# Kernel tuning notes

Hardware: AMD Instinct MI355X
Metric: run time of the kernel (lower is better)

## Reference

```python
import jax, jax.numpy as jnp
import numpy as np

B, S = 512, 256          # batch, seq_len
C, H = 8, 16             # num_cells, expert hidden size
M = 20                   # memory_size (hard-coded in module)
NT = C * H               # num_trajectories = 128
ENC_IN = M * (NT + 1)    # 20*129 = 2580, memory_encode input dim
A_H = 16                 # agent LSTM hidden


def setup_inputs() -> dict:
    key = jax.random.key(0)
    ks = jax.random.split(key, 20)
    r = lambda i, shape: 0.1 * jax.random.normal(ks[i], shape, dtype=jnp.float32)
    return {
        "x": jax.random.normal(ks[0], (B, S, 1), dtype=jnp.float32),
        "pred0": jax.random.uniform(ks[1], (B, 1), dtype=jnp.float32),
        "gate0": jax.nn.softmax(jax.random.uniform(ks[2], (B, C), dtype=jnp.float32), axis=1),
        # experts: C parallel LSTM cells (input 1, hidden H) + per-cell scalar head
        "W_ih": r(3, (C, 4 * H, 1)), "W_hh": r(4, (C, 4 * H, H)),
        "b_ih": r(5, (C, 4 * H)), "b_hh": r(6, (C, 4 * H)),
        "W_o": r(7, (C, H)), "b_o": r(8, (C,)),
        # memory_encode: Linear(2580,64) ReLU Linear(64,16) ReLU
        "W1": r(9, (64, ENC_IN)), "b1": r(10, (64,)),
        "W2": r(11, (16, 64)), "b2": r(12, (16,)),
        # gate_linear: Linear(16, C) + softmax
        "Wg": r(13, (C, 16)), "bg": r(14, (C,)),
        # agent: 2 stacked LSTM cells (16 -> 16)
        "Wa_ih": r(15, (2, 4 * A_H, A_H)), "Wa_hh": r(16, (2, 4 * A_H, A_H)),
        "ba_ih": r(17, (2, 4 * A_H)), "ba_hh": r(18, (2, 4 * A_H)),
    }


def _cell(z, c):
    # PyTorch LSTMCell gate order: i, f, g, o
    i, f, g, o = jnp.split(z, 4, axis=-1)
    c2 = jax.nn.sigmoid(f) * c + jax.nn.sigmoid(i) * jnp.tanh(g)
    return jax.nn.sigmoid(o) * jnp.tanh(c2), c2


def reference(x, pred0, gate0, W_ih, W_hh, b_ih, b_hh, W_o, b_o,
              W1, b1, W2, b2, Wg, bg, Wa_ih, Wa_hh, ba_ih, ba_hh):
    mem0 = jnp.zeros((B, M, NT + 1), jnp.float32).at[:, :, -1].set(0.5)
    eh0 = jnp.zeros((B, H), jnp.float32)   # combined expert h (shared across cells)
    a0 = jnp.zeros((2, B, A_H), jnp.float32)

    def step(carry, x_t):
        mem, eh, ec, pred, gate_state, ah, ac = carry
        error = x_t - pred                                        # [B,1]
        # experts: C LSTM cells, all reading the shared combined state
        z = (jnp.einsum('bf,cgf->bcg', x_t, W_ih)
             + jnp.einsum('bh,cgh->bcg', eh, W_hh)
             + b_ih + b_hh)                                       # [B,C,4H]
        nh, nc = _cell(z, ec[:, None, :])                          # [B,C,H]
        o = jnp.einsum('bch,ch->bc', nh, W_o) + b_o               # [B,C]
        # memory_step: matmul(mstep, mem) shifts rows down by 1, row 0 <- w
        w = jnp.concatenate([nh.reshape(B, -1), error], axis=1)   # [B,NT+1]
        mem = jnp.concatenate([w[:, None, :], mem[:, :-1, :]], axis=1)
        # memory_encode MLP
        e1 = jax.nn.relu(mem.reshape(B, -1) @ W1.T + b1)
        ai = jax.nn.relu(e1 @ W2.T + b2)                           # [B,16]
        # agent: 2 stacked LSTM cells
        ah_l, ac_l, inp_l = [], [], ai
        for l in range(2):
            zl = inp_l @ Wa_ih[l].T + ba_ih[l] + ah[l] @ Wa_hh[l].T + ba_hh[l]
            hl, cl = _cell(zl, ac[l])
            ah_l.append(hl); ac_l.append(cl)
            inp_l = hl
        ah2, ac2 = jnp.stack(ah_l), jnp.stack(ac_l)
        gate = jax.nn.softmax(inp_l @ Wg.T + bg, axis=1)           # [B,C]
        # theta = clip(2.5 * mean|mem[:, :10, -1]|, 0, 1)  (relu(t)-relu(t-1))
        theta = jnp.clip(jnp.mean(jnp.abs(mem[:, :10, -1]), axis=1) * 2.5, 0.0, 1.0)[:, None]
        gate = gate * theta + gate_state * (1.0 - theta)
        eh2 = jnp.einsum('bc,bch->bh', gate, nh)                   # bmm(gate, h)
        ec2 = jnp.einsum('bc,bch->bh', gate, nc)
        pred2 = jnp.einsum('bc,bc->b', gate, o)[:, None]           # [B,1]
        return (mem, eh2, ec2, pred2, gate, ah2, ac2), pred2

    xs = jnp.swapaxes(x, 0, 1)  # [S,B,1]
    _, preds = jax.lax.scan(step, (mem0, eh0, eh0, pred0, gate0, a0, a0), xs)
    return jnp.swapaxes(preds, 0, 1)  # [B,S,1]
```

## Files before the change

kernel.cpp:

```cpp
#include <hip/hip_runtime.h>
#include <math.h>

#define S_LEN 256
#define NCELL 8
#define HID 16
#define MEM 20
#define NB 4
#define NTHR 512

typedef _Float16 v8h __attribute__((ext_vector_type(8)));
typedef float v4f __attribute__((ext_vector_type(4)));

__device__ __forceinline__ float sigm(float v) { return 1.0f / (1.0f + __expf(-v)); }
__device__ __forceinline__ float tanh_f(float v) { return 1.0f - 2.0f / (__expf(2.0f * v) + 1.0f); }
__device__ __forceinline__ float dot4(float4 a, float4 b) {
    return fmaf(a.x, b.x, fmaf(a.y, b.y, fmaf(a.z, b.z, a.w * b.w)));
}
__device__ __forceinline__ v4f mfma16(v8h a, v8h b, v4f c) {
    return __builtin_amdgcn_mfma_f32_16x16x32_f16(a, b, c, 0, 0, 0);
}

__global__ __launch_bounds__(256)
void prep_w1(const float* __restrict__ W1, _Float16* __restrict__ W1F) {
    int idx = blockIdx.x * 256 + threadIdx.x;
    if (idx < MEM * 4 * 4 * 64 * 8) {
        int e = idx & 7;
        int lane = (idx >> 3) & 63;
        int jt = (idx >> 9) & 3;
        int t = idx >> 11;
        int m = t >> 2, kc = t & 3;
        int j = jt * 16 + (lane & 15);
        int k = kc * 32 + (lane >> 4) * 8 + e;
        W1F[idx] = (_Float16)W1[j * 2580 + m * 129 + k];
    }
}

#define E1P(BB, V) { \
    V = b1_l[lane] \
      + red[par][1][BB][lane] + red[par][2][BB][lane] + red[par][3][BB][lane] \
      + red[par][4][BB][lane] + red[par][5][BB][lane] + red[par][6][BB][lane] \
      + red[par][7][BB][lane]; \
    int sl_ = head; \
    _Pragma("unroll") \
    for (int m_ = 0; m_ < MEM; ++m_) { \
        V = fmaf(Werr_l[m_ * 64 + lane], errS[BB][sl_], V); \
        ++sl_; if (sl_ >= MEM) sl_ = 0; } }

#define E1F(BB, V) { \
    V += red0[0][BB][lane] + red0[1][BB][lane] + red0[2][BB][lane] + red0[3][BB][lane]; \
    e1S[BB][lane] = fmaxf(V, 0.f); }

__global__ __attribute__((amdgpu_flat_work_group_size(NTHR, NTHR)))
void mmoe_kernel(const float* __restrict__ x, const float* __restrict__ pred0,
                 const float* __restrict__ gate0,
                 const float* __restrict__ W_ih, const float* __restrict__ W_hh,
                 const float* __restrict__ b_ih, const float* __restrict__ b_hh,
                 const float* __restrict__ W_o, const float* __restrict__ b_o,
                 const float* __restrict__ W1, const float* __restrict__ b1,
                 const float* __restrict__ W2, const float* __restrict__ b2,
                 const float* __restrict__ Wg, const float* __restrict__ bg,
                 const float* __restrict__ Wa_ih, const float* __restrict__ Wa_hh,
                 const float* __restrict__ ba_ih, const float* __restrict__ ba_hh,
                 const _Float16* __restrict__ W1F,
                 float* __restrict__ out)
{
    __shared__ __align__(16) _Float16 ringH[NB][MEM][128];
    __shared__ float errS[NB][MEM];
    __shared__ __align__(16) float Whh_l[512 * 20];
    __shared__ float Wih_l[512], bias_l[512];
    __shared__ __align__(16) float WaI[2][64 * 20], WaH[2][64 * 20];
    __shared__ float ba_l[2][64];
    __shared__ __align__(16) float W2_l[16 * 68];
    __shared__ float b2_l[16];
    __shared__ __align__(16) float Wg_l[8][16], Wo_l[8][16];
    __shared__ float bg_l[8], bo_l[8];
    __shared__ float Werr_l[MEM * 64];
    __shared__ float b1_l[64];
    __shared__ float xS[NB][S_LEN];
    __shared__ __align__(16) float ehS[NB][HID], ecS[NB][HID];
    __shared__ __align__(16) float nhS[NB][NCELL][HID], ncS[NB][NCELL][HID];
    __shared__ float oS[NB][NCELL], predS[NB], gateS[NB][NCELL];
    __shared__ __align__(16) float ahS[2][NB][HID], acS[2][NB][HID];
    __shared__ __align__(16) float e1S[NB][64], aiS[NB][HID];
    __shared__ __align__(16) float glog[NB][8];
    __shared__ __align__(16) float red[2][8][NB][64];
    __shared__ __align__(16) float red0[4][NB][64];

    const int tid = threadIdx.x;
    const int b0 = blockIdx.x * NB;
    const int lane = tid & 63, wv = tid >> 6;
    const int quad = lane >> 4, nn = lane & 15, bb4 = nn & 3;

    for (int i = tid; i < 512 * 16; i += NTHR) { int g = i >> 4, q = i & 15; Whh_l[g * 20 + q] = W_hh[i]; }
    for (int i = tid; i < 512; i += NTHR) { Wih_l[i] = W_ih[i]; bias_l[i] = b_ih[i] + b_hh[i]; }
    for (int i = tid; i < 2048; i += NTHR) {
        int l = i >> 10, r = i & 1023, g = r >> 4, q = r & 15;
        WaI[l][g * 20 + q] = Wa_ih[i]; WaH[l][g * 20 + q] = Wa_hh[i];
    }
    for (int i = tid; i < 128; i += NTHR) { int l = i >> 6, g = i & 63; ba_l[l][g] = ba_ih[i] + ba_hh[i]; }
    for (int i = tid; i < 1024; i += NTHR) { int r = i >> 6, q = i & 63; W2_l[r * 68 + q] = W2[i]; }
    for (int i = tid; i < 1280; i += NTHR) { int m = i >> 6, j = i & 63; Werr_l[i] = W1[j * 2580 + m * 129 + 128]; }
    if (tid < 64) b1_l[tid] = b1[tid];
    if (tid < 16) b2_l[tid] = b2[tid];
    if (tid < 128) { int c = tid >> 4, h = tid & 15; Wg_l[c][h] = Wg[tid]; Wo_l[c][h] = W_o[tid]; }
    if (tid < 8) { bg_l[tid] = bg[tid]; bo_l[tid] = b_o[tid]; }
    for (int i = tid; i < NB * S_LEN; i += NTHR) { int b = i >> 8, s = i & 255; xS[b][s] = x[(b0 + b) * S_LEN + s]; }
    for (int i = tid; i < NB * MEM * 128; i += NTHR) ((_Float16*)ringH)[i] = (_Float16)0.0f;
    for (int i = tid; i < 2 * 8 * NB * 64; i += NTHR) ((float*)red)[i] = 0.0f;
    if (tid < NB * MEM) { int b = tid / MEM, m = tid % MEM; errS[b][m] = 0.5f; }
    if (tid < NB * HID) {
        int b = tid >> 4, h = tid & 15;
        ehS[b][h] = 0.f; ecS[b][h] = 0.f;
        ahS[0][b][h] = 0.f; ahS[1][b][h] = 0.f;
        acS[0][b][h] = 0.f; acS[1][b][h] = 0.f;
    }
    if (tid < NB) predS[tid] = pred0[b0 + tid];
    if (tid < NB * NCELL) { int b = tid >> 3, c = tid & 7; gateS[b][c] = gate0[(b0 + b) * NCELL + c]; }
    __syncthreads();

    const v8h* Wb = (const v8h*)W1F;

    int head = 0;
    #pragma unroll 1
    for (int t = 0; t < S_LEN; ++t) {
        head = (head == 0) ? (MEM - 1) : (head - 1);
        const int par = t & 1, np = par ^ 1;
        float v0, v1, v2, v3;

        {
            int b = tid >> 7, c = (tid >> 4) & 7, h = tid & 15;
            float xv = xS[b][t];
            const float4* ep = (const float4*)&ehS[b][0];
            float4 e0 = ep[0], e1v = ep[1], e2 = ep[2], e3 = ep[3];
            float zg[4];
            #pragma unroll
            for (int gi = 0; gi < 4; ++gi) {
                int g = c * 64 + gi * 16 + h;
                const float* wr = &Whh_l[g * 20];
                float z = bias_l[g] + xv * Wih_l[g];
                z += dot4(e0, *(const float4*)&wr[0]) + dot4(e1v, *(const float4*)&wr[4])
                   + dot4(e2, *(const float4*)&wr[8]) + dot4(e3, *(const float4*)&wr[12]);
                zg[gi] = z;
            }
            float cc = ecS[b][h];
            float c2 = sigm(zg[1]) * cc + sigm(zg[0]) * tanh_f(zg[2]);
            float hv = sigm(zg[3]) * tanh_f(c2);
            nhS[b][c][h] = hv; ncS[b][c][h] = c2;
            ringH[b][head][c * 16 + h] = (_Float16)hv;
            if (tid < NB) errS[tid][head] = xS[tid][t] - predS[tid];
        }
        __syncthreads();

        {
            int kc = wv >> 1, jt0 = (wv & 1) * 2;
            v8h bfrag = *(const v8h*)&ringH[bb4][head][kc * 32 + quad * 8];
            v8h a0 = Wb[(size_t)(kc * 4 + jt0) * 64 + lane];
            v8h a1 = Wb[(size_t)(kc * 4 + jt0 + 1) * 64 + lane];
            v4f c0 = {0.f, 0.f, 0.f, 0.f}, c1 = {0.f, 0.f, 0.f, 0.f};
            c0 = mfma16(a0, bfrag, c0);
            c1 = mfma16(a1, bfrag, c1);
            if (nn < 4) {
                *(v4f*)&red0[kc][nn][jt0 * 16 + quad * 4] = c0;
                *(v4f*)&red0[kc][nn][(jt0 + 1) * 16 + quad * 4] = c1;
            }
            if (wv == 0) { E1P(0, v0) E1P(1, v1) E1P(2, v2) E1P(3, v3) }
        }
        __syncthreads();

        if (wv >= 1) {
            int kt = (wv - 1) * 11;
            int ktEnd = kt + 11; if (ktEnd > 76) ktEnd = 76;
            v4f c0 = {0.f,0.f,0.f,0.f}, c1 = {0.f,0.f,0.f,0.f};
            v4f c2 = {0.f,0.f,0.f,0.f}, c3 = {0.f,0.f,0.f,0.f};
            size_t tb = (size_t)(4 + kt) * 256 + lane;
            v8h pA0 = Wb[tb], pA1 = Wb[tb + 64], pA2 = Wb[tb + 128], pA3 = Wb[tb + 192];
            int m0 = 1 + (kt >> 2), kc0 = kt & 3;
            int sl0 = head + m0 - 1; if (sl0 >= MEM) sl0 -= MEM;
            v8h pB = *(const v8h*)&ringH[bb4][sl0][kc0 * 32 + quad * 8];
            #pragma unroll 1
            for (; kt < ktEnd; ++kt) {
                v8h A0 = pA0, A1 = pA1, A2 = pA2, A3 = pA3, B = pB;
                int kn = kt + 1;
                if (kn < ktEnd) {
                    size_t tn = (size_t)(4 + kn) * 256 + lane;
                    pA0 = Wb[tn]; pA1 = Wb[tn + 64]; pA2 = Wb[tn + 128]; pA3 = Wb[tn + 192];
                    int mn = 1 + (kn >> 2), kcn = kn & 3;
                    int sn = head + mn - 1; if (sn >= MEM) sn -= MEM;
                    pB = *(const v8h*)&ringH[bb4][sn][kcn * 32 + quad * 8];
                }
                c0 = mfma16(A0, B, c0);
                c1 = mfma16(A1, B, c1);
                c2 = mfma16(A2, B, c2);
                c3 = mfma16(A3, B, c3);
            }
            if (nn < 4) {
                *(v4f*)&red[np][wv][nn][ 0 + quad * 4] = c0;
                *(v4f*)&red[np][wv][nn][16 + quad * 4] = c1;
                *(v4f*)&red[np][wv][nn][32 + quad * 4] = c2;
                *(v4f*)&red[np][wv][nn][48 + quad * 4] = c3;
            }
        } else {
            E1F(0, v0) E1F(1, v1) E1F(2, v2) E1F(3, v3)
            const int j = lane;
            {
                int bb = j >> 4, i = j & 15;
                const float4* epq = (const float4*)&e1S[bb][0];
                float s = b2_l[i];
                #pragma unroll
                for (int q = 0; q < 16; ++q) s += dot4(*(const float4*)&W2_l[i * 68 + q * 4], epq[q]);
                aiS[bb][i] = fmaxf(s, 0.f);
            }
            if (j < 32) {
                int bb = j >> 3, c = j & 7;
                const float4* np_ = (const float4*)&nhS[bb][c][0];
                const float4* wp = (const float4*)&Wo_l[c][0];
                float s = bo_l[c];
                #pragma unroll
                for (int q4 = 0; q4 < 4; ++q4) s += dot4(np_[q4], wp[q4]);
                oS[bb][c] = s;
            }
            #pragma unroll
            for (int l = 0; l < 2; ++l) {
                int bb = j >> 4, h = j & 15;
                const float4* ip = (l == 0) ? (const float4*)&aiS[bb][0]
                                            : (const float4*)&ahS[0][bb][0];
                const float4* hp = (const float4*)&ahS[l][bb][0];
                float4 i0 = ip[0], i1 = ip[1], i2 = ip[2], i3 = ip[3];
                float4 h0 = hp[0], h1 = hp[1], h2v = hp[2], h3 = hp[3];
                float zg[4];
                #pragma unroll
                for (int gi = 0; gi < 4; ++gi) {
                    int g = gi * 16 + h;
                    const float* wi = &WaI[l][g * 20];
                    const float* wh = &WaH[l][g * 20];
                    float z = ba_l[l][g];
                    z += dot4(i0, *(const float4*)&wi[0]) + dot4(i1, *(const float4*)&wi[4])
                       + dot4(i2, *(const float4*)&wi[8]) + dot4(i3, *(const float4*)&wi[12]);
                    z += dot4(h0, *(const float4*)&wh[0]) + dot4(h1, *(const float4*)&wh[4])
                       + dot4(h2v, *(const float4*)&wh[8]) + dot4(h3, *(const float4*)&wh[12]);
                    zg[gi] = z;
                }
                float c2 = sigm(zg[1]) * acS[l][bb][h] + sigm(zg[0]) * tanh_f(zg[2]);
                acS[l][bb][h] = c2;
                ahS[l][bb][h] = sigm(zg[3]) * tanh_f(c2);
            }
            if (j < 32) {
                int bb = j >> 3, c = j & 7;
                const float4* hp = (const float4*)&ahS[1][bb][0];
                const float4* wg = (const float4*)&Wg_l[c][0];
                float s = bg_l[c];
                #pragma unroll
                for (int q = 0; q < 4; ++q) s += dot4(wg[q], hp[q]);
                glog[bb][c] = s;
                float4 ga = *(const float4*)&glog[bb][0];
                float4 gb = *(const float4*)&glog[bb][4];
                float mx = fmaxf(fmaxf(fmaxf(ga.x, ga.y), fmaxf(ga.z, ga.w)),
                                 fmaxf(fmaxf(gb.x, gb.y), fmaxf(gb.z, gb.w)));
                float sum = __expf(ga.x - mx) + __expf(ga.y - mx) + __expf(ga.z - mx) + __expf(ga.w - mx)
                          + __expf(gb.x - mx) + __expf(gb.y - mx) + __expf(gb.z - mx) + __expf(gb.w - mx);
                float p = __expf(s - mx) / sum;
                float th = 0.f;
                #pragma unroll
                for (int m = 0; m < 10; ++m) {
                    int sl = head + m; if (sl >= MEM) sl -= MEM;
                    th += fabsf(errS[bb][sl]);
                }
                th *= 0.25f;
                th = fminf(fmaxf(th, 0.f), 1.f);
                gateS[bb][c] = p * th + gateS[bb][c] * (1.f - th);
            }
            {
                int bb = j >> 4, h = j & 15;
                float se = 0.f, sc = 0.f;
                #pragma unroll
                for (int c = 0; c < 8; ++c) {
                    float g = gateS[bb][c];
                    se = fmaf(g, nhS[bb][c][h], se);
                    sc = fmaf(g, ncS[bb][c][h], sc);
                }
                ehS[bb][h] = se; ecS[bb][h] = sc;
            }
            if (j < NB) {
                float s = 0.f;
                #pragma unroll
                for (int c = 0; c < 8; ++c) s = fmaf(gateS[j][c], oS[j][c], s);
                predS[j] = s;
                out[(b0 + j) * S_LEN + t] = s;
            }
        }
        __syncthreads();
    }
}

extern "C" void kernel_launch(void* const* d_in, const int* in_sizes, int n_in,
                              void* d_out, int out_size, void* d_ws, size_t ws_size,
                              hipStream_t stream) {
    const float* xp    = (const float*)d_in[0];
    const float* pred0 = (const float*)d_in[1];
    const float* gate0 = (const float*)d_in[2];
    const float* W_ih  = (const float*)d_in[3];
    const float* W_hh  = (const float*)d_in[4];
    const float* b_ih  = (const float*)d_in[5];
    const float* b_hh  = (const float*)d_in[6];
    const float* W_o   = (const float*)d_in[7];
    const float* b_o   = (const float*)d_in[8];
    const float* W1    = (const float*)d_in[9];
    const float* b1    = (const float*)d_in[10];
    const float* W2    = (const float*)d_in[11];
    const float* b2    = (const float*)d_in[12];
    const float* Wg    = (const float*)d_in[13];
    const float* bg    = (const float*)d_in[14];
    const float* Wa_ih = (const float*)d_in[15];
    const float* Wa_hh = (const float*)d_in[16];
    const float* ba_ih = (const float*)d_in[17];
    const float* ba_hh = (const float*)d_in[18];
    _Float16* W1F = (_Float16*)d_ws;

    prep_w1<<<(MEM * 4 * 4 * 64 * 8 + 255) / 256, 256, 0, stream>>>(W1, W1F);
    mmoe_kernel<<<512 / NB, NTHR, 0, stream>>>(
        xp, pred0, gate0, W_ih, W_hh, b_ih, b_hh, W_o, b_o,
        W1, b1, W2, b2, Wg, bg, Wa_ih, Wa_hh, ba_ih, ba_hh,
        W1F, (float*)d_out);
}
```

Baseline: 1.294 ms.

## Rebalance per-step work across waves and deepen W1 prefetch pipeline

Result: slower. 1.333 ms (+3.1%).

```diff
diff --git a/kernel.cpp b/kernel.cpp
--- a/kernel.cpp
+++ b/kernel.cpp
@@ -7,6 +7,7 @@
 #define MEM 20
 #define NB 4
 #define NTHR 512
+#define RSTR 2592
 
 typedef _Float16 v8h __attribute__((ext_vector_type(8)));
 typedef float v4f __attribute__((ext_vector_type(4)));
@@ -19,6 +20,8 @@
 __device__ __forceinline__ v4f mfma16(v8h a, v8h b, v4f c) {
     return __builtin_amdgcn_mfma_f32_16x16x32_f16(a, b, c, 0, 0, 0);
 }
+
+#define RING(b, s, k) ringH[(b) * RSTR + (s) * 128 + (k)]
 
 __global__ __launch_bounds__(256)
 void prep_w1(const float* __restrict__ W1, _Float16* __restrict__ W1F) {
@@ -39,15 +42,11 @@
     V = b1_l[lane] \
       + red[par][1][BB][lane] + red[par][2][BB][lane] + red[par][3][BB][lane] \
       + red[par][4][BB][lane] + red[par][5][BB][lane] + red[par][6][BB][lane] \
-      + red[par][7][BB][lane]; \
-    int sl_ = head; \
-    _Pragma("unroll") \
-    for (int m_ = 0; m_ < MEM; ++m_) { \
-        V = fmaf(Werr_l[m_ * 64 + lane], errS[BB][sl_], V); \
-        ++sl_; if (sl_ >= MEM) sl_ = 0; } }
+      + red[par][7][BB][lane]; }
 
 #define E1F(BB, V) { \
-    V += red0[0][BB][lane] + red0[1][BB][lane] + red0[2][BB][lane] + red0[3][BB][lane]; \
+    V += errdotS[BB][lane] \
+       + red0[0][BB][lane] + red0[1][BB][lane] + red0[2][BB][lane] + red0[3][BB][lane]; \
     e1S[BB][lane] = fmaxf(V, 0.f); }
 
 __global__ __attribute__((amdgpu_flat_work_group_size(NTHR, NTHR)))
@@ -64,7 +63,8 @@
                  const _Float16* __restrict__ W1F,
                  float* __restrict__ out)
 {
-    __shared__ __align__(16) _Float16 ringH[NB][MEM][128];
+    __shared__ __align__(16) _Float16 ringH[NB * RSTR];
+    __shared__ __align__(16) _Float16 W10F_l[8192];
     __shared__ float errS[NB][MEM];
     __shared__ __align__(16) float Whh_l[512 * 20];
     __shared__ float Wih_l[512], bias_l[512];
@@ -85,6 +85,8 @@
     __shared__ __align__(16) float glog[NB][8];
     __shared__ __align__(16) float red[2][8][NB][64];
     __shared__ __align__(16) float red0[4][NB][64];
+    __shared__ float errdotS[NB][64];
+    __shared__ float thS[NB];
 
     const int tid = threadIdx.x;
     const int b0 = blockIdx.x * NB;
@@ -100,12 +102,13 @@
     for (int i = tid; i < 128; i += NTHR) { int l = i >> 6, g = i & 63; ba_l[l][g] = ba_ih[i] + ba_hh[i]; }
     for (int i = tid; i < 1024; i += NTHR) { int r = i >> 6, q = i & 63; W2_l[r * 68 + q] = W2[i]; }
     for (int i = tid; i < 1280; i += NTHR) { int m = i >> 6, j = i & 63; Werr_l[i] = W1[j * 2580 + m * 129 + 128]; }
+    for (int i = tid; i < 8192; i += NTHR) W10F_l[i] = W1F[i];
     if (tid < 64) b1_l[tid] = b1[tid];
     if (tid < 16) b2_l[tid] = b2[tid];
     if (tid < 128) { int c = tid >> 4, h = tid & 15; Wg_l[c][h] = Wg[tid]; Wo_l[c][h] = W_o[tid]; }
     if (tid < 8) { bg_l[tid] = bg[tid]; bo_l[tid] = b_o[tid]; }
     for (int i = tid; i < NB * S_LEN; i += NTHR) { int b = i >> 8, s = i & 255; xS[b][s] = x[(b0 + b) * S_LEN + s]; }
-    for (int i = tid; i < NB * MEM * 128; i += NTHR) ((_Float16*)ringH)[i] = (_Float16)0.0f;
+    for (int i = tid; i < NB * RSTR; i += NTHR) ringH[i] = (_Float16)0.0f;
     for (int i = tid; i < 2 * 8 * NB * 64; i += NTHR) ((float*)red)[i] = 0.0f;
     if (tid < NB * MEM) { int b = tid / MEM, m = tid % MEM; errS[b][m] = 0.5f; }
     if (tid < NB * HID) {
@@ -119,6 +122,7 @@
     __syncthreads();
 
     const v8h* Wb = (const v8h*)W1F;
+    const v8h* WL = (const v8h*)W10F_l;
 
     int head = 0;
     #pragma unroll 1
@@ -146,24 +150,57 @@
             float c2 = sigm(zg[1]) * cc + sigm(zg[0]) * tanh_f(zg[2]);
             float hv = sigm(zg[3]) * tanh_f(c2);
             nhS[b][c][h] = hv; ncS[b][c][h] = c2;
-            ringH[b][head][c * 16 + h] = (_Float16)hv;
+            RING(b, head, c * 16 + h) = (_Float16)hv;
             if (tid < NB) errS[tid][head] = xS[tid][t] - predS[tid];
         }
         __syncthreads();
 
         {
             int kc = wv >> 1, jt0 = (wv & 1) * 2;
-            v8h bfrag = *(const v8h*)&ringH[bb4][head][kc * 32 + quad * 8];
-            v8h a0 = Wb[(size_t)(kc * 4 + jt0) * 64 + lane];
-            v8h a1 = Wb[(size_t)(kc * 4 + jt0 + 1) * 64 + lane];
-            v4f c0 = {0.f, 0.f, 0.f, 0.f}, c1 = {0.f, 0.f, 0.f, 0.f};
-            c0 = mfma16(a0, bfrag, c0);
-            c1 = mfma16(a1, bfrag, c1);
+            v8h bfrag = *(const v8h*)&RING(bb4, head, kc * 32 + quad * 8);
+            v8h a0 = WL[(kc * 4 + jt0) * 64 + lane];
+            v8h a1 = WL[(kc * 4 + jt0 + 1) * 64 + lane];
+            v4f z = {0.f, 0.f, 0.f, 0.f};
+            v4f c0 = mfma16(a0, bfrag, z);
+            v4f c1 = mfma16(a1, bfrag, z);
             if (nn < 4) {
                 *(v4f*)&red0[kc][nn][jt0 * 16 + quad * 4] = c0;
                 *(v4f*)&red0[kc][nn][(jt0 + 1) * 16 + quad * 4] = c1;
             }
-            if (wv == 0) { E1P(0, v0) E1P(1, v1) E1P(2, v2) E1P(3, v3) }
+            if (wv == 0) {
+                E1P(0, v0) E1P(1, v1) E1P(2, v2) E1P(3, v3)
+            } else if (wv == 1) {
+                if (lane < 32) {
+                    int bb = lane >> 3, c = lane & 7;
+                    const float4* np_ = (const float4*)&nhS[bb][c][0];
+                    const float4* wp = (const float4*)&Wo_l[c][0];
+                    float s = bo_l[c];
+                    #pragma unroll
+                    for (int q4 = 0; q4 < 4; ++q4) s += dot4(np_[q4], wp[q4]);
+                    oS[bb][c] = s;
+                }
+            } else if (wv == 2) {
+                if (lane < NB) {
+                    float th = 0.f;
+                    #pragma unroll
+                    for (int m = 0; m < 10; ++m) {
+                        int sl = head + m; if (sl >= MEM) sl -= MEM;
+                        th += fabsf(errS[lane][sl]);
+                    }
+                    th *= 0.25f;
+                    thS[lane] = fminf(fmaxf(th, 0.f), 1.f);
+                }
+            } else if (wv >= 3 && wv < 7) {
+                int bb = wv - 3;
+                float s = 0.f;
+                int sl = head;
+                #pragma unroll
+                for (int m = 0; m < MEM; ++m) {
+                    s = fmaf(Werr_l[m * 64 + lane], errS[bb][sl], s);
+                    ++sl; if (sl >= MEM) sl = 0;
+                }
+                errdotS[bb][lane] = s;
+            }
         }
         __syncthreads();
 
@@ -172,26 +209,32 @@
             int ktEnd = kt + 11; if (ktEnd > 76) ktEnd = 76;
             v4f c0 = {0.f,0.f,0.f,0.f}, c1 = {0.f,0.f,0.f,0.f};
             v4f c2 = {0.f,0.f,0.f,0.f}, c3 = {0.f,0.f,0.f,0.f};
-            size_t tb = (size_t)(4 + kt) * 256 + lane;
-            v8h pA0 = Wb[tb], pA1 = Wb[tb + 64], pA2 = Wb[tb + 128], pA3 = Wb[tb + 192];
+            size_t t0 = (size_t)(4 + kt) * 256 + lane;
+            v8h aA0 = Wb[t0], aA1 = Wb[t0 + 64], aA2 = Wb[t0 + 128], aA3 = Wb[t0 + 192];
             int m0 = 1 + (kt >> 2), kc0 = kt & 3;
-            int sl0 = head + m0 - 1; if (sl0 >= MEM) sl0 -= MEM;
-            v8h pB = *(const v8h*)&ringH[bb4][sl0][kc0 * 32 + quad * 8];
+            int s0 = head + m0 - 1; if (s0 >= MEM) s0 -= MEM;
+            v8h aB = *(const v8h*)&RING(bb4, s0, kc0 * 32 + quad * 8);
+            size_t t1 = t0 + 256;
+            v8h bA0 = Wb[t1], bA1 = Wb[t1 + 64], bA2 = Wb[t1 + 128], bA3 = Wb[t1 + 192];
+            int k1 = kt + 1, m1 = 1 + (k1 >> 2), kc1 = k1 & 3;
+            int s1 = head + m1 - 1; if (s1 >= MEM) s1 -= MEM;
+            v8h bB = *(const v8h*)&RING(bb4, s1, kc1 * 32 + quad * 8);
             #pragma unroll 1
-            for (; kt < ktEnd; ++kt) {
-                v8h A0 = pA0, A1 = pA1, A2 = pA2, A3 = pA3, B = pB;
-                int kn = kt + 1;
+            for (int i = kt; i < ktEnd; ++i) {
+                v8h uA0 = aA0, uA1 = aA1, uA2 = aA2, uA3 = aA3, uB = aB;
+                aA0 = bA0; aA1 = bA1; aA2 = bA2; aA3 = bA3; aB = bB;
+                int kn = i + 2;
                 if (kn < ktEnd) {
                     size_t tn = (size_t)(4 + kn) * 256 + lane;
-                    pA0 = Wb[tn]; pA1 = Wb[tn + 64]; pA2 = Wb[tn + 128]; pA3 = Wb[tn + 192];
+                    bA0 = Wb[tn]; bA1 = Wb[tn + 64]; bA2 = Wb[tn + 128]; bA3 = Wb[tn + 192];
                     int mn = 1 + (kn >> 2), kcn = kn & 3;
                     int sn = head + mn - 1; if (sn >= MEM) sn -= MEM;
-                    pB = *(const v8h*)&ringH[bb4][sn][kcn * 32 + quad * 8];
-                }
-                c0 = mfma16(A0, B, c0);
-                c1 = mfma16(A1, B, c1);
-                c2 = mfma16(A2, B, c2);
-                c3 = mfma16(A3, B, c3);
+                    bB = *(const v8h*)&RING(bb4, sn, kcn * 32 + quad * 8);
+                }
+                c0 = mfma16(uA0, uB, c0);
+                c1 = mfma16(uA1, uB, c1);
+                c2 = mfma16(uA2, uB, c2);
+                c3 = mfma16(uA3, uB, c3);
             }
             if (nn < 4) {
                 *(v4f*)&red[np][wv][nn][ 0 + quad * 4] = c0;
@@ -209,15 +252,6 @@
                 #pragma unroll
                 for (int q = 0; q < 16; ++q) s += dot4(*(const float4*)&W2_l[i * 68 + q * 4], epq[q]);
                 aiS[bb][i] = fmaxf(s, 0.f);
-            }
-            if (j < 32) {
-                int bb = j >> 3, c = j & 7;
-                const float4* np_ = (const float4*)&nhS[bb][c][0];
-                const float4* wp = (const float4*)&Wo_l[c][0];
-                float s = bo_l[c];
-                #pragma unroll
-                for (int q4 = 0; q4 < 4; ++q4) s += dot4(np_[q4], wp[q4]);
-                oS[bb][c] = s;
             }
             #pragma unroll
             for (int l = 0; l < 2; ++l) {
@@ -259,14 +293,7 @@
                 float sum = __expf(ga.x - mx) + __expf(ga.y - mx) + __expf(ga.z - mx) + __expf(ga.w - mx)
                           + __expf(gb.x - mx) + __expf(gb.y - mx) + __expf(gb.z - mx) + __expf(gb.w - mx);
                 float p = __expf(s - mx) / sum;
-                float th = 0.f;
-                #pragma unroll
-                for (int m = 0; m < 10; ++m) {
-                    int sl = head + m; if (sl >= MEM) sl -= MEM;
-                    th += fabsf(errS[bb][sl]);
-                }
-                th *= 0.25f;
-                th = fminf(fmaxf(th, 0.f), 1.f);
+                float th = thS[bb];
                 gateS[bb][c] = p * th + gateS[bb][c] * (1.f - th);
             }
             {
```
